# Kernel tuning notes

Measured on AMD Instinct MI355X. Metric: run time of the kernel, lower is better.

Reference implementation:

```python
import jax, jax.numpy as jnp
import numpy as np

N = 50000  # nodes
E = 1600000  # directed edges
F_IN = 64
H = 64
C = 16
EPS = 1e-12


def setup_inputs() -> dict:
    key = jax.random.key(0)
    ks = jax.random.split(key, 10)
    x = jax.random.normal(ks[0], (N, F_IN), jnp.float32)
    edge_index = jax.random.randint(ks[1], (2, E), 0, N, dtype=jnp.int32)
    def lin(k, fan_in, fan_out):
        return jax.random.normal(k, (fan_in, fan_out), jnp.float32) * (1.0 / np.sqrt(fan_in))
    return {
        "x": x,
        "edge_index": edge_index,
        "W1": lin(ks[2], F_IN, H), "b1": jnp.zeros((H,), jnp.float32),
        "W2": lin(ks[3], H, H),    "b2": jnp.zeros((H,), jnp.float32),
        "W3": lin(ks[4], H, H),    "b3": jnp.zeros((H,), jnp.float32),
        "Wlin": lin(ks[5], 3 * H, C), "blin": jnp.zeros((C,), jnp.float32),
    }


def _gcn_norm(edge_index, n):
    # add self loops, compute symmetric GCN normalization D^-1/2 (A+I) D^-1/2
    loop = jnp.arange(n, dtype=edge_index.dtype)
    row = jnp.concatenate([edge_index[0], loop])  # target nodes
    col = jnp.concatenate([edge_index[1], loop])  # source nodes
    deg = jax.ops.segment_sum(jnp.ones_like(row, dtype=jnp.float32), row, num_segments=n)
    dis = jnp.where(deg > 0, jax.lax.rsqrt(jnp.maximum(deg, 1.0)), 0.0)
    norm = dis[row] * dis[col]  # [E+N]
    return row, col, norm


def _gcn_layer(x, row, col, norm, W, b):
    h = x @ W                              # [N, H]
    msg = h[col] * norm[:, None]           # gather sources, scale
    agg = jax.ops.segment_sum(msg, row, num_segments=x.shape[0])  # scatter-add
    return agg + b


def _l2norm(x):
    # torch F.normalize(p=2, dim=1)
    n = jnp.sqrt(jnp.sum(x * x, axis=1, keepdims=True))
    return x / jnp.maximum(n, EPS)


def reference(x, edge_index, W1, b1, W2, b2, W3, b3, Wlin, blin):
    row, col, norm = _gcn_norm(edge_index, x.shape[0])
    stack = []
    h = x
    for (W, b) in ((W1, b1), (W2, b2), (W3, b3)):
        h = _gcn_layer(h, row, col, norm, W, b)
        h = jax.nn.relu(h)
        h = _l2norm(h)
        stack.append(h)
    emb = jnp.concatenate(stack, axis=1)   # [N, 3H]
    out = emb @ Wlin + blin                # [N, C]
    return jax.nn.log_softmax(out, axis=1)
```

## Files before the change

kernel.cpp:

```cpp
#include <hip/hip_runtime.h>
#include <hip/hip_bf16.h>

#define NN 50000
#define EE 1600000
#define NB 391
#define CAPB 4608
#define CPAD 16
#define EPB 4096
#define BCAP 28

typedef __attribute__((ext_vector_type(8))) short short8;
typedef __attribute__((ext_vector_type(4))) float floatx4;

__device__ __forceinline__ float ldext(const void* p, long i, int f32) {
    return f32 ? ((const float*)p)[i]
               : __bfloat162float(((const __hip_bfloat16*)p)[i]);
}

__device__ __forceinline__ float b2f(unsigned short u) {
    unsigned int x = ((unsigned int)u) << 16;
    float f; __builtin_memcpy(&f, &x, 4); return f;
}
__device__ __forceinline__ unsigned short f2b(float f) {
    __hip_bfloat16 h = __float2bfloat16(f);
    unsigned short u; __builtin_memcpy(&u, &h, 2); return u;
}
__device__ __forceinline__ float asf(unsigned int x) {
    float f; __builtin_memcpy(&f, &x, 4); return f;
}

__global__ void k_bucket(const int* __restrict__ row, const int* __restrict__ col,
                         int* __restrict__ bcur, unsigned int* __restrict__ bdata,
                         const unsigned short* __restrict__ xu, int* __restrict__ flag) {
    __shared__ int lcnt[NB];
    __shared__ unsigned binned[NB * BCAP];
    __shared__ int dcnt;
    int tid = threadIdx.x;
    if (blockIdx.x == 0) {
        if (tid == 0) dcnt = 0;
        __syncthreads();
        int local = 0;
        for (int j = 0; j < 16; ++j) {
            unsigned short u = xu[2 * (tid + 256 * j)];
            int ex = (u >> 7) & 0xFF;
            if (ex == 0xFF || ex < 0x60) local++;
        }
        atomicAdd(&dcnt, local);
        __syncthreads();
        if (tid == 0) flag[0] = (dcnt > 256) ? 1 : 0;
    }
    long base = (long)blockIdx.x * EPB;
    int nedge = (int)min((long)EPB, (long)EE - base);
    for (int k = tid; k < NB; k += 256) lcnt[k] = 0;
    __syncthreads();
    const int4* r4 = (const int4*)(row + base);
    const int4* c4 = (const int4*)(col + base);
    for (int j = tid; j < (nedge >> 2); j += 256) {
        int4 rr = r4[j], cc = c4[j];
        #pragma unroll
        for (int t = 0; t < 4; ++t) {
            int r = (&rr.x)[t], c = (&cc.x)[t];
            int b = r >> 7;
            unsigned rec = ((unsigned)(r & 127) << 16) | (unsigned)c;
            int p = atomicAdd(&lcnt[b], 1);
            if (p < BCAP) binned[b * BCAP + p] = rec;
            else {
                int gp = atomicAdd(&bcur[b * CPAD], 1);
                if (gp < CAPB) bdata[(long)b * CAPB + gp] = rec;
            }
        }
    }
    __syncthreads();
    for (int b = tid; b < NB; b += 256) {
        int n = min(lcnt[b], BCAP);
        if (!n) continue;
        int gb = atomicAdd(&bcur[b * CPAD], n);
        long dst = (long)b * CAPB;
        for (int j = 0; j < n; ++j)
            if (gb + j < CAPB) bdata[dst + gb + j] = binned[b * BCAP + j];
    }
}

__global__ void k_csr(const int* __restrict__ bcur, const unsigned* __restrict__ bdata,
                      int* __restrict__ row_ptr, float* __restrict__ dis,
                      unsigned short* __restrict__ csr_col) {
    __shared__ unsigned recs[CAPB];
    __shared__ int cnt[128];
    __shared__ int incl[128];
    __shared__ int curs[128];
    __shared__ int redu[4];
    int b = blockIdx.x, tid = threadIdx.x;
    int lane = tid & 63, wid = tid >> 6;
    int part = 0;
    for (int j = tid; j < b; j += 256) part += min(bcur[j * CPAD], CAPB);
    #pragma unroll
    for (int off = 32; off; off >>= 1) part += __shfl_xor(part, off);
    if (lane == 0) redu[wid] = part;
    if (tid < 128) cnt[tid] = 0;
    __syncthreads();
    int base = redu[0] + redu[1] + redu[2] + redu[3];
    int n = min(bcur[b * CPAD], CAPB);
    const unsigned* dp = bdata + (long)b * CAPB;
    for (int i = tid; i < n; i += 256) {
        unsigned rec = dp[i];
        recs[i] = rec;
        atomicAdd(&cnt[(rec >> 16) & 127], 1);
    }
    __syncthreads();
    if (tid < 128) {
        int x = cnt[tid];
        #pragma unroll
        for (int off = 1; off < 64; off <<= 1) {
            int y = __shfl_up(x, off);
            if (lane >= off) x += y;
        }
        incl[tid] = x;
    }
    __syncthreads();
    int r0 = b << 7;
    if (tid < 128) {
        int ic = incl[tid] + (wid == 1 ? incl[63] : 0);
        int excl = base + ic - cnt[tid];
        curs[tid] = excl;
        int r = r0 + tid;
        if (r <= NN) row_ptr[r] = excl;
        if (r < NN) dis[r] = rsqrtf((float)(cnt[tid] + 1));
    }
    __syncthreads();
    for (int i = tid; i < n; i += 256) {
        unsigned rec = recs[i];
        int p = atomicAdd(&curs[(rec >> 16) & 127], 1);
        csr_col[p] = (unsigned short)(rec & 0xFFFF);
    }
}

template <bool EXT>
__global__ void k_gemm(const void* __restrict__ X, const void* __restrict__ W,
                       const int* __restrict__ flag, const float* __restrict__ dis,
                       unsigned short* __restrict__ Hout) {
    __shared__ __align__(16) unsigned short xs[64 * 72];
    int tid = threadIdx.x;
    int n0 = blockIdx.x * 64;
    const int f32 = flag[0];
    for (int idx = tid; idx < 4096; idx += 256) {
        int nn = idx >> 6, k = idx & 63;
        int n = n0 + nn;
        unsigned short v = 0;
        if (n < NN) {
            long ofs = (long)n * 64 + k;
            if (EXT) v = f32 ? f2b(((const float*)X)[ofs]) : ((const unsigned short*)X)[ofs];
            else     v = ((const unsigned short*)X)[ofs];
        }
        xs[nn * 72 + k] = v;
    }
    __syncthreads();
    int lane = tid & 63, wid = tid >> 6;
    int m0 = wid * 16;
    int quad = lane >> 4, nl = lane & 15;
    short8 a0 = *(const short8*)(xs + (m0 + nl) * 72 + quad * 8);
    short8 a1 = *(const short8*)(xs + (m0 + nl) * 72 + quad * 8 + 32);
    floatx4 acc[4];
    const unsigned short* Wb = (const unsigned short*)W;
    const float* Wf = (const float*)W;
    #pragma unroll
    for (int ct = 0; ct < 4; ++ct) {
        short8 b0, b1;
        int n = ct * 16 + nl;
        #pragma unroll
        for (int j = 0; j < 8; ++j) {
            int k0 = quad * 8 + j;
            b0[j] = (short)(f32 ? f2b(Wf[k0 * 64 + n]) : Wb[k0 * 64 + n]);
            b1[j] = (short)(f32 ? f2b(Wf[(k0 + 32) * 64 + n]) : Wb[(k0 + 32) * 64 + n]);
        }
        floatx4 c = {0.f, 0.f, 0.f, 0.f};
        c = __builtin_amdgcn_mfma_f32_16x16x32_bf16(a0, b0, c, 0, 0, 0);
        c = __builtin_amdgcn_mfma_f32_16x16x32_bf16(a1, b1, c, 0, 0, 0);
        acc[ct] = c;
    }
    #pragma unroll
    for (int r = 0; r < 4; ++r) {
        int node = n0 + m0 + quad * 4 + r;
        if (node < NN) {
            float dn = dis[node];
            #pragma unroll
            for (int ct = 0; ct < 4; ++ct)
                Hout[(long)node * 64 + ct * 16 + nl] = f2b(dn * acc[ct][r]);
        }
    }
}

__global__ void k_agg(const uint4* __restrict__ hp128, const int* __restrict__ row_ptr,
                      const unsigned short* __restrict__ csr_col,
                      const float* __restrict__ dis, const void* __restrict__ bias,
                      const int* __restrict__ flag,
                      unsigned short* __restrict__ eo ) {
    int lane = threadIdx.x & 63, wid = threadIdx.x >> 6;
    int half = lane >> 5;
    int i = blockIdx.x * 8 + wid * 2 + half;
    bool valid = (i < NN);
    int iv = valid ? i : 0;
    int q4 = (lane >> 3) & 3;
    int fl = lane & 7;
    float2 A0 = {0,0}, A1 = {0,0}, A2 = {0,0}, A3 = {0,0};
    #define ADDU(u) do { \
        A0.x += asf((u).x << 16); A0.y += asf((u).x & 0xFFFF0000u); \
        A1.x += asf((u).y << 16); A1.y += asf((u).y & 0xFFFF0000u); \
        A2.x += asf((u).z << 16); A2.y += asf((u).z & 0xFFFF0000u); \
        A3.x += asf((u).w << 16); A3.y += asf((u).w & 0xFFFF0000u); } while (0)
    if (valid && q4 == 0) {
        uint4 u = hp128[(long)iv * 8 + fl];
        ADDU(u);
    }
    int e  = valid ? row_ptr[iv] : 0;
    int e1 = valid ? row_ptr[iv + 1] : 0;
    while (e + 15 < e1) {
        int c0 = csr_col[e + q4];
        int c1 = csr_col[e + 4 + q4];
        int c2 = csr_col[e + 8 + q4];
        int c3 = csr_col[e + 12 + q4];
        uint4 u0 = hp128[(long)c0 * 8 + fl];
        uint4 u1 = hp128[(long)c1 * 8 + fl];
        uint4 u2 = hp128[(long)c2 * 8 + fl];
        uint4 u3 = hp128[(long)c3 * 8 + fl];
        ADDU(u0); ADDU(u1); ADDU(u2); ADDU(u3);
        e += 16;
    }
    if (e + 7 < e1) {
        int c0 = csr_col[e + q4];
        int c1 = csr_col[e + 4 + q4];
        uint4 u0 = hp128[(long)c0 * 8 + fl];
        uint4 u1 = hp128[(long)c1 * 8 + fl];
        ADDU(u0); ADDU(u1);
        e += 8;
    }
    if (e + 3 < e1) {
        int c = csr_col[e + q4];
        uint4 u = hp128[(long)c * 8 + fl];
        ADDU(u);
        e += 4;
    }
    int rem = e1 - e;
    if (q4 < rem) {
        int c = csr_col[e + q4];
        uint4 u = hp128[(long)c * 8 + fl];
        ADDU(u);
    }
    #undef ADDU
    #pragma unroll
    for (int off = 8; off < 32; off <<= 1) {
        A0.x += __shfl_xor(A0.x, off); A0.y += __shfl_xor(A0.y, off);
        A1.x += __shfl_xor(A1.x, off); A1.y += __shfl_xor(A1.y, off);
        A2.x += __shfl_xor(A2.x, off); A2.y += __shfl_xor(A2.y, off);
        A3.x += __shfl_xor(A3.x, off); A3.y += __shfl_xor(A3.y, off);
    }
    const int f32 = flag[0];
    float di = dis[iv];
    float v0 = fmaf(di, A0.x, ldext(bias, 8 * fl + 0, f32));
    float v1 = fmaf(di, A0.y, ldext(bias, 8 * fl + 1, f32));
    float v2 = fmaf(di, A1.x, ldext(bias, 8 * fl + 2, f32));
    float v3 = fmaf(di, A1.y, ldext(bias, 8 * fl + 3, f32));
    float v4 = fmaf(di, A2.x, ldext(bias, 8 * fl + 4, f32));
    float v5 = fmaf(di, A2.y, ldext(bias, 8 * fl + 5, f32));
    float v6 = fmaf(di, A3.x, ldext(bias, 8 * fl + 6, f32));
    float v7 = fmaf(di, A3.y, ldext(bias, 8 * fl + 7, f32));
    v0 = fmaxf(v0, 0.f); v1 = fmaxf(v1, 0.f); v2 = fmaxf(v2, 0.f); v3 = fmaxf(v3, 0.f);
    v4 = fmaxf(v4, 0.f); v5 = fmaxf(v5, 0.f); v6 = fmaxf(v6, 0.f); v7 = fmaxf(v7, 0.f);
    float s = fmaf(v0, v0, fmaf(v1, v1, fmaf(v2, v2, v3 * v3)))
            + fmaf(v4, v4, fmaf(v5, v5, fmaf(v6, v6, v7 * v7)));
    #pragma unroll
    for (int off = 4; off; off >>= 1) s += __shfl_xor(s, off);
    float inv = 1.f / fmaxf(sqrtf(s), 1e-12f);
    if (valid && q4 == 0) {
        union { unsigned short us[8]; uint4 v; } pk;
        pk.us[0] = f2b(v0 * inv); pk.us[1] = f2b(v1 * inv);
        pk.us[2] = f2b(v2 * inv); pk.us[3] = f2b(v3 * inv);
        pk.us[4] = f2b(v4 * inv); pk.us[5] = f2b(v5 * inv);
        pk.us[6] = f2b(v6 * inv); pk.us[7] = f2b(v7 * inv);
        *(uint4*)(eo + (long)i * 64 + 8 * fl) = pk.v;
    }
}

__global__ void k_out(const unsigned short* __restrict__ emb, const void* __restrict__ Wlin,
                      const void* __restrict__ blin, const int* __restrict__ flag,
                      void* __restrict__ out) {
    int tid = threadIdx.x, lane = tid & 63, wid = tid >> 6;
    int quad = lane >> 4, nl = lane & 15;
    int base = blockIdx.x * 64 + wid * 16;
    const int f32 = flag[0];
    const unsigned short* Wb = (const unsigned short*)Wlin;
    const float* Wf = (const float*)Wlin;
    int ia = min(base + nl, NN - 1);
    floatx4 c = {0.f, 0.f, 0.f, 0.f};
    #pragma unroll
    for (int kc = 0; kc < 6; ++kc) {
        short8 b;
        #pragma unroll
        for (int j = 0; j < 8; ++j) {
            int k = kc * 32 + quad * 8 + j;
            b[j] = (short)(f32 ? f2b(Wf[k * 16 + nl]) : Wb[k * 16 + nl]);
        }
        int L = kc >> 1, ko = (kc & 1) * 32 + quad * 8;
        short8 a = *(const short8*)(emb + (long)L * NN * 64 + (long)ia * 64 + ko);
        c = __builtin_amdgcn_mfma_f32_16x16x32_bf16(a, b, c, 0, 0, 0);
    }
    float bl = ldext(blin, nl, f32);
    #pragma unroll
    for (int r = 0; r < 4; ++r) {
        float v = c[r] + bl;
        float m = v;
        #pragma unroll
        for (int off = 1; off < 16; off <<= 1) m = fmaxf(m, __shfl_xor(m, off));
        float ex = __expf(v - m);
        float s = ex;
        #pragma unroll
        for (int off = 1; off < 16; off <<= 1) s += __shfl_xor(s, off);
        float o = (v - m) - __logf(s);
        int node = base + quad * 4 + r;
        if (node < NN) {
            long oidx = (long)node * 16 + nl;
            if (f32) ((float*)out)[oidx] = o;
            else     ((__hip_bfloat16*)out)[oidx] = __float2bfloat16(o);
        }
    }
}

extern "C" void kernel_launch(void* const* d_in, const int* in_sizes, int n_in,
                              void* d_out, int out_size, void* d_ws, size_t ws_size,
                              hipStream_t stream) {
    const void* x    = d_in[0];
    const int*  ei   = (const int*)d_in[1];
    const void* W1   = d_in[2];
    const void* b1   = d_in[3];
    const void* W2   = d_in[4];
    const void* b2   = d_in[5];
    const void* W3   = d_in[6];
    const void* b3   = d_in[7];
    const void* Wlin = d_in[8];
    const void* blin = d_in[9];

    unsigned short* h   = (unsigned short*)d_ws;
    unsigned short* emb = h + (long)NN * 64;
    float* dis     = (float*)(emb + (long)3 * NN * 64);
    int*   row_ptr = (int*)(dis + NN);
    int*   flag    = row_ptr + NN + 64;
    int*   bcur    = flag + 16;
    unsigned* bdata = (unsigned*)(bcur + NB * CPAD);
    unsigned short* csr_col = (unsigned short*)(bdata + (long)NB * CAPB);

    const int* row = ei;
    const int* col = ei + EE;

    (void)hipMemsetAsync(bcur, 0, NB * CPAD * sizeof(int), stream);
    k_bucket<<<(EE + EPB - 1) / EPB, 256, 0, stream>>>(row, col, bcur, bdata,
                                                       (const unsigned short*)x, flag);
    k_csr<<<NB, 256, 0, stream>>>(bcur, bdata, row_ptr, dis, csr_col);

    int gb = (NN + 63) / 64;
    int ga = (NN + 7) / 8;
    const uint4* hp128 = (const uint4*)h;
    k_gemm<true><<<gb, 256, 0, stream>>>(x, W1, flag, dis, h);
    k_agg<<<ga, 256, 0, stream>>>(hp128, row_ptr, csr_col, dis, b1, flag, emb);
    k_gemm<false><<<gb, 256, 0, stream>>>(emb, W2, flag, dis, h);
    k_agg<<<ga, 256, 0, stream>>>(hp128, row_ptr, csr_col, dis, b2, flag, emb + (long)NN * 64);
    k_gemm<false><<<gb, 256, 0, stream>>>(emb + (long)NN * 64, W3, flag, dis, h);
    k_agg<<<ga, 256, 0, stream>>>(hp128, row_ptr, csr_col, dis, b3, flag, emb + (long)2 * NN * 64);

    k_out<<<gb, 256, 0, stream>>>(emb, Wlin, blin, flag, d_out);
}
```

Before: 287.0 us.

## Split hidden features into two 32-wide planes and aggregate each half separately

```diff
diff --git a/kernel.cpp b/kernel.cpp
--- a/kernel.cpp
+++ b/kernel.cpp
@@ -183,13 +183,15 @@
         if (node < NN) {
             float dn = dis[node];
             #pragma unroll
-            for (int ct = 0; ct < 4; ++ct)
-                Hout[(long)node * 64 + ct * 16 + nl] = f2b(dn * acc[ct][r]);
-        }
-    }
-}
-
-__global__ void k_agg(const uint4* __restrict__ hp128, const int* __restrict__ row_ptr,
+            for (int ct = 0; ct < 4; ++ct) {
+                long po = (ct >> 1) ? (long)NN * 32 : 0;
+                Hout[po + (long)node * 32 + (ct & 1) * 16 + nl] = f2b(dn * acc[ct][r]);
+            }
+        }
+    }
+}
+
+__global__ void k_agg(const uint4* __restrict__ hp, const int* __restrict__ row_ptr,
                       const unsigned short* __restrict__ csr_col,
                       const float* __restrict__ dis, const void* __restrict__ bias,
                       const int* __restrict__ flag,
@@ -199,84 +201,110 @@
     int i = blockIdx.x * 8 + wid * 2 + half;
     bool valid = (i < NN);
     int iv = valid ? i : 0;
-    int q4 = (lane >> 3) & 3;
-    int fl = lane & 7;
-    float2 A0 = {0,0}, A1 = {0,0}, A2 = {0,0}, A3 = {0,0};
-    #define ADDU(u) do { \
-        A0.x += asf((u).x << 16); A0.y += asf((u).x & 0xFFFF0000u); \
-        A1.x += asf((u).y << 16); A1.y += asf((u).y & 0xFFFF0000u); \
-        A2.x += asf((u).z << 16); A2.y += asf((u).z & 0xFFFF0000u); \
-        A3.x += asf((u).w << 16); A3.y += asf((u).w & 0xFFFF0000u); } while (0)
-    if (valid && q4 == 0) {
-        uint4 u = hp128[(long)iv * 8 + fl];
-        ADDU(u);
-    }
-    int e  = valid ? row_ptr[iv] : 0;
+    int q8 = (lane >> 2) & 7;
+    int fl = lane & 3;
+    const uint4* hpA = hp;
+    const uint4* hpB = hp + (long)NN * 4;
+    #define ADD8(u, A) do { \
+        A[0] += asf((u).x << 16); A[1] += asf((u).x & 0xFFFF0000u); \
+        A[2] += asf((u).y << 16); A[3] += asf((u).y & 0xFFFF0000u); \
+        A[4] += asf((u).z << 16); A[5] += asf((u).z & 0xFFFF0000u); \
+        A[6] += asf((u).w << 16); A[7] += asf((u).w & 0xFFFF0000u); } while (0)
+    float a[8], b[8];
+    #pragma unroll
+    for (int j = 0; j < 8; ++j) { a[j] = 0.f; b[j] = 0.f; }
+    int e0 = valid ? row_ptr[iv] : 0;
     int e1 = valid ? row_ptr[iv + 1] : 0;
-    while (e + 15 < e1) {
-        int c0 = csr_col[e + q4];
-        int c1 = csr_col[e + 4 + q4];
-        int c2 = csr_col[e + 8 + q4];
-        int c3 = csr_col[e + 12 + q4];
-        uint4 u0 = hp128[(long)c0 * 8 + fl];
-        uint4 u1 = hp128[(long)c1 * 8 + fl];
-        uint4 u2 = hp128[(long)c2 * 8 + fl];
-        uint4 u3 = hp128[(long)c3 * 8 + fl];
-        ADDU(u0); ADDU(u1); ADDU(u2); ADDU(u3);
-        e += 16;
-    }
-    if (e + 7 < e1) {
-        int c0 = csr_col[e + q4];
-        int c1 = csr_col[e + 4 + q4];
-        uint4 u0 = hp128[(long)c0 * 8 + fl];
-        uint4 u1 = hp128[(long)c1 * 8 + fl];
-        ADDU(u0); ADDU(u1);
-        e += 8;
-    }
-    if (e + 3 < e1) {
-        int c = csr_col[e + q4];
-        uint4 u = hp128[(long)c * 8 + fl];
-        ADDU(u);
-        e += 4;
-    }
-    int rem = e1 - e;
-    if (q4 < rem) {
-        int c = csr_col[e + q4];
-        uint4 u = hp128[(long)c * 8 + fl];
-        ADDU(u);
-    }
-    #undef ADDU
-    #pragma unroll
-    for (int off = 8; off < 32; off <<= 1) {
-        A0.x += __shfl_xor(A0.x, off); A0.y += __shfl_xor(A0.y, off);
-        A1.x += __shfl_xor(A1.x, off); A1.y += __shfl_xor(A1.y, off);
-        A2.x += __shfl_xor(A2.x, off); A2.y += __shfl_xor(A2.y, off);
-        A3.x += __shfl_xor(A3.x, off); A3.y += __shfl_xor(A3.y, off);
+    if (valid && q8 == 0) {
+        uint4 u = hpA[(long)iv * 4 + fl];
+        ADD8(u, a);
+    }
+    {
+        int e = e0;
+        while (e + 15 < e1) {
+            int c0 = (int)__builtin_nontemporal_load(csr_col + e + q8);
+            int c1 = (int)__builtin_nontemporal_load(csr_col + e + 8 + q8);
+            uint4 u0 = hpA[(long)c0 * 4 + fl];
+            uint4 u1 = hpA[(long)c1 * 4 + fl];
+            ADD8(u0, a); ADD8(u1, a);
+            e += 16;
+        }
+        if (e + 7 < e1) {
+            int c0 = (int)__builtin_nontemporal_load(csr_col + e + q8);
+            uint4 u0 = hpA[(long)c0 * 4 + fl];
+            ADD8(u0, a);
+            e += 8;
+        }
+        int rem = e1 - e;
+        if (q8 < rem) {
+            int c0 = (int)__builtin_nontemporal_load(csr_col + e + q8);
+            uint4 u0 = hpA[(long)c0 * 4 + fl];
+            ADD8(u0, a);
+        }
+    }
+    if (valid && q8 == 0) {
+        uint4 u = hpB[(long)iv * 4 + fl];
+        ADD8(u, b);
+    }
+    {
+        int e = e0;
+        while (e + 15 < e1) {
+            int c0 = (int)__builtin_nontemporal_load(csr_col + e + q8);
+            int c1 = (int)__builtin_nontemporal_load(csr_col + e + 8 + q8);
+            uint4 u0 = hpB[(long)c0 * 4 + fl];
+            uint4 u1 = hpB[(long)c1 * 4 + fl];
+            ADD8(u0, b); ADD8(u1, b);
+            e += 16;
+        }
+        if (e + 7 < e1) {
+            int c0 = (int)__builtin_nontemporal_load(csr_col + e + q8);
+            uint4 u0 = hpB[(long)c0 * 4 + fl];
+            ADD8(u0, b);
+            e += 8;
+        }
+        int rem = e1 - e;
+        if (q8 < rem) {
+            int c0 = (int)__builtin_nontemporal_load(csr_col + e + q8);
+            uint4 u0 = hpB[(long)c0 * 4 + fl];
+            ADD8(u0, b);
+        }
+    }
+    #undef ADD8
+    #pragma unroll
+    for (int off = 4; off < 32; off <<= 1) {
+        #pragma unroll
+        for (int j = 0; j < 8; ++j) {
+            a[j] += __shfl_xor(a[j], off);
+            b[j] += __shfl_xor(b[j], off);
+        }
     }
     const int f32 = flag[0];
     float di = dis[iv];
-    float v0 = fmaf(di, A0.x, ldext(bias, 8 * fl + 0, f32));
-    float v1 = fmaf(di, A0.y, ldext(bias, 8 * fl + 1, f32));
-    float v2 = fmaf(di, A1.x, ldext(bias, 8 * fl + 2, f32));
-    float v3 = fmaf(di, A1.y, ldext(bias, 8 * fl + 3, f32));
-    float v4 = fmaf(di, A2.x, ldext(bias, 8 * fl + 4, f32));
-    float v5 = fmaf(di, A2.y, ldext(bias, 8 * fl + 5, f32));
-    float v6 = fmaf(di, A3.x, ldext(bias, 8 * fl + 6, f32));
-    float v7 = fmaf(di, A3.y, ldext(bias, 8 * fl + 7, f32));
-    v0 = fmaxf(v0, 0.f); v1 = fmaxf(v1, 0.f); v2 = fmaxf(v2, 0.f); v3 = fmaxf(v3, 0.f);
-    v4 = fmaxf(v4, 0.f); v5 = fmaxf(v5, 0.f); v6 = fmaxf(v6, 0.f); v7 = fmaxf(v7, 0.f);
-    float s = fmaf(v0, v0, fmaf(v1, v1, fmaf(v2, v2, v3 * v3)))
-            + fmaf(v4, v4, fmaf(v5, v5, fmaf(v6, v6, v7 * v7)));
-    #pragma unroll
-    for (int off = 4; off; off >>= 1) s += __shfl_xor(s, off);
+    float vA[8], vB[8];
+    float s = 0.f;
+    #pragma unroll
+    for (int j = 0; j < 8; ++j) {
+        float x0 = fmaf(di, a[j], ldext(bias, fl * 8 + j, f32));
+        float x1 = fmaf(di, b[j], ldext(bias, 32 + fl * 8 + j, f32));
+        x0 = fmaxf(x0, 0.f); x1 = fmaxf(x1, 0.f);
+        vA[j] = x0; vB[j] = x1;
+        s = fmaf(x0, x0, s);
+        s = fmaf(x1, x1, s);
+    }
+    #pragma unroll
+    for (int off = 1; off < 4; off <<= 1) s += __shfl_xor(s, off);
     float inv = 1.f / fmaxf(sqrtf(s), 1e-12f);
-    if (valid && q4 == 0) {
+    if (valid && q8 == 0) {
         union { unsigned short us[8]; uint4 v; } pk;
-        pk.us[0] = f2b(v0 * inv); pk.us[1] = f2b(v1 * inv);
-        pk.us[2] = f2b(v2 * inv); pk.us[3] = f2b(v3 * inv);
-        pk.us[4] = f2b(v4 * inv); pk.us[5] = f2b(v5 * inv);
-        pk.us[6] = f2b(v6 * inv); pk.us[7] = f2b(v7 * inv);
+        #pragma unroll
+        for (int j = 0; j < 8; ++j) pk.us[j] = f2b(vA[j] * inv);
         *(uint4*)(eo + (long)i * 64 + 8 * fl) = pk.v;
+    }
+    if (valid && q8 == 1) {
+        union { unsigned short us[8]; uint4 v; } pk;
+        #pragma unroll
+        for (int j = 0; j < 8; ++j) pk.us[j] = f2b(vB[j] * inv);
+        *(uint4*)(eo + (long)i * 64 + 32 + 8 * fl) = pk.v;
     }
 }
 
@@ -357,13 +385,13 @@
 
     int gb = (NN + 63) / 64;
     int ga = (NN + 7) / 8;
-    const uint4* hp128 = (const uint4*)h;
+    const uint4* hp = (const uint4*)h;
     k_gemm<true><<<gb, 256, 0, stream>>>(x, W1, flag, dis, h);
-    k_agg<<<ga, 256, 0, stream>>>(hp128, row_ptr, csr_col, dis, b1, flag, emb);
+    k_agg<<<ga, 256, 0, stream>>>(hp, row_ptr, csr_col, dis, b1, flag, emb);
     k_gemm<false><<<gb, 256, 0, stream>>>(emb, W2, flag, dis, h);
-    k_agg<<<ga, 256, 0, stream>>>(hp128, row_ptr, csr_col, dis, b2, flag, emb + (long)NN * 64);
+    k_agg<<<ga, 256, 0, stream>>>(hp, row_ptr, csr_col, dis, b2, flag, emb + (long)NN * 64);
     k_gemm<false><<<gb, 256, 0, stream>>>(emb + (long)NN * 64, W3, flag, dis, h);
-    k_agg<<<ga, 256, 0, stream>>>(hp128, row_ptr, csr_col, dis, b3, flag, emb + (long)2 * NN * 64);
+    k_agg<<<ga, 256, 0, stream>>>(hp, row_ptr, csr_col, dis, b3, flag, emb + (long)2 * NN * 64);
 
     k_out<<<gb, 256, 0, stream>>>(emb, Wlin, blin, flag, d_out);
 }
```

New measurement: 331.3 us. +15.4%, slower.
